# Kernel optimization log

Measured on AMD Instinct MI355X. Metric: run time of the kernel, lower is better.

## Reference

```python
import jax, jax.numpy as jnp
import numpy as np
import math

EMBED_DIM = 1024
NUM_HEADS = 16
PROJ_DIM = 1024
HEAD_DIM = PROJ_DIM // NUM_HEADS  # 64
ALPHA = 0.3  # warmup_steps=0, step_count irrelevant -> alpha_eff = alpha
DIFFUSION_STEPS = 2


def setup_inputs() -> dict:
    key = jax.random.key(0)
    ks = jax.random.split(key, 9)
    B, N, D = 1, 2048, EMBED_DIM
    s_in = 1.0 / math.sqrt(D)
    s_p = 1.0 / math.sqrt(PROJ_DIM)
    return {
        "hidden_states": jax.random.normal(ks[0], (B, N, D), dtype=jnp.float32),
        # Linear weights stored as [in, out] (apply as x @ W + b)
        "Wq": jax.random.normal(ks[1], (D, PROJ_DIM), dtype=jnp.float32) * s_in,
        "bq": jax.random.normal(ks[2], (PROJ_DIM,), dtype=jnp.float32) * s_in,
        "Wk": jax.random.normal(ks[3], (D, PROJ_DIM), dtype=jnp.float32) * s_in,
        "bk": jax.random.normal(ks[4], (PROJ_DIM,), dtype=jnp.float32) * s_in,
        "Wv": jax.random.normal(ks[5], (D, PROJ_DIM), dtype=jnp.float32) * s_in,
        "bv": jax.random.normal(ks[6], (PROJ_DIM,), dtype=jnp.float32) * s_in,
        "Wo": jax.random.normal(ks[7], (PROJ_DIM, D), dtype=jnp.float32) * s_p,
        "bo": jax.random.normal(ks[8], (D,), dtype=jnp.float32) * s_p,
    }


def reference(hidden_states, Wq, bq, Wk, bk, Wv, bv, Wo, bo):
    B, N, D = hidden_states.shape
    H, hd = NUM_HEADS, HEAD_DIM

    def split_heads(x):  # [B, N, P] -> [B, H, N, hd]
        return x.reshape(B, -1, H, hd).transpose(0, 2, 1, 3)

    Q = split_heads(hidden_states @ Wq + bq)
    K = split_heads(hidden_states @ Wk + bk)
    V = split_heads(hidden_states @ Wv + bv)

    # scores: note original uses (sqrt(hd) + 1e-8) denominator here
    scores = jnp.einsum("bhqd,bhkd->bhqk", Q, K) / (math.sqrt(hd) + 1e-8)
    p0 = jax.nn.softmax(scores, axis=-1)

    # key-transition matrix P: exact sqrt(hd) denominator
    sim = jnp.einsum("bhid,bhjd->bhij", K, K) / math.sqrt(hd)
    P = jax.nn.softmax(sim, axis=-1)

    # iterative diffusion, unrolled (early-stop can only fire after the
    # final update when diffusion_steps=2, so output is identical)
    a = ALPHA
    p = p0
    for _ in range(DIFFUSION_STEPS):
        p = (1.0 - a) * p0 + a * jnp.einsum("bhqn,bhnm->bhqm", p, P)

    attn = jnp.einsum("bhqk,bhkd->bhqd", p, V)
    attn = attn.transpose(0, 2, 1, 3).reshape(B, N, PROJ_DIM)
    out = attn @ Wo + bo
    return out, p
```

## Files before the change

### kernel.cpp

```cpp
#include <hip/hip_runtime.h>


typedef __attribute__((ext_vector_type(8))) short bf16x8;
typedef __attribute__((ext_vector_type(4))) short s16x4;
typedef __attribute__((ext_vector_type(4))) float f32x4;

constexpr int N_TOK   = 2048;
constexpr int N_HEADS = 16;
constexpr int HD      = 64;
constexpr int EMB     = 1024;

#define DEVINL __device__ __forceinline__

DEVINL unsigned short f2bf_u(float f) {
  unsigned x = __float_as_uint(f);
  return (unsigned short)((x + 0x7fffu + ((x >> 16) & 1u)) >> 16);
}
DEVINL float bf2f_u(unsigned short h) { return __uint_as_float(((unsigned)h) << 16); }

DEVINL void async16(const void* src, void* dst) {
  __builtin_amdgcn_global_load_lds(
      (const __attribute__((address_space(1))) void*)src,
      (__attribute__((address_space(3))) void*)dst, 16, 0, 0);
}

enum : int { EPI_F32SCALE = 0, EPI_F32BIAS, EPI_BF16, EPI_QKSPLIT, EPI_VSPLIT,
             EPI_DIFF_BF16, EPI_DIFF_F32 };

template<int EPI>
__global__ __launch_bounds__(512, 2)
void gemm256_diff(const unsigned short* __restrict__ Am, int lda, long long sAz,
                  const unsigned short* __restrict__ Bm, int ldb, long long sBz,
                  int K,
                  const unsigned short* __restrict__ P0, int ldp0, long long sPz,
                  void* __restrict__ Cv, int ldc, long long sCz)
{
  __shared__ __align__(16) char smem[2 * 65536];
  const int tid  = threadIdx.x;
  const int lane = tid & 63, wv = tid >> 6;
  const int wr = wv >> 2, wc = wv & 3;
  const int l15 = lane & 15, g = lane >> 4;
  const int z = blockIdx.z;
  const size_t brow = (size_t)blockIdx.y * 256;
  const size_t bcol = (size_t)blockIdx.x * 256;
  const unsigned short* Ab = Am + (size_t)z * (size_t)sAz;
  const unsigned short* Bb = Bm + (size_t)z * (size_t)sBz;
  const int NT = K >> 6;

  const int cbs = (tid & 7) * 16;
  const int r00 = (tid >> 3),       r01 = 64  + (tid >> 3);
  const int r10 = 128 + (tid >> 3), r11 = 192 + (tid >> 3);
  const char* sA00 = (const char*)Ab + ((brow + r00) * (size_t)lda) * 2 + (cbs ^ ((r00 & 7) << 4));
  const char* sA01 = (const char*)Ab + ((brow + r01) * (size_t)lda) * 2 + (cbs ^ ((r01 & 7) << 4));
  const char* sA10 = (const char*)Ab + ((brow + r10) * (size_t)lda) * 2 + (cbs ^ ((r10 & 7) << 4));
  const char* sA11 = (const char*)Ab + ((brow + r11) * (size_t)lda) * 2 + (cbs ^ ((r11 & 7) << 4));
  const char* sB00 = (const char*)Bb + ((bcol + r00) * (size_t)ldb) * 2 + (cbs ^ ((r00 & 7) << 4));
  const char* sB01 = (const char*)Bb + ((bcol + r01) * (size_t)ldb) * 2 + (cbs ^ ((r01 & 7) << 4));
  const char* sB10 = (const char*)Bb + ((bcol + r10) * (size_t)ldb) * 2 + (cbs ^ ((r10 & 7) << 4));
  const char* sB11 = (const char*)Bb + ((bcol + r11) * (size_t)ldb) * 2 + (cbs ^ ((r11 & 7) << 4));

  f32x4 acc[8][4];
  #pragma unroll
  for (int m = 0; m < 8; ++m)
    #pragma unroll
    for (int n = 0; n < 4; ++n) acc[m][n] = f32x4{0.f, 0.f, 0.f, 0.f};

  auto ldA = [&](int cur, int mf, int kk) -> bf16x8 {
    const int row = wr * 128 + mf * 16 + l15;
    const int c = (kk * 64 + g * 16) ^ ((row & 7) << 4);
    return *(const bf16x8*)(smem + cur * 65536 + row * 128 + c);
  };
  auto ldB = [&](int cur, int nf, int kk) -> bf16x8 {
    const int row = wc * 64 + nf * 16 + l15;
    const int c = (kk * 64 + g * 16) ^ ((row & 7) << 4);
    return *(const bf16x8*)(smem + cur * 65536 + 32768 + row * 128 + c);
  };

  {
    char* d0 = smem;
    async16(sA00, d0 +             wv * 1024);
    async16(sA01, d0 +  8192 +     wv * 1024);
    async16(sA10, d0 + 16384 +     wv * 1024);
    async16(sA11, d0 + 24576 +     wv * 1024);
    async16(sB00, d0 + 32768 +     wv * 1024);
    async16(sB01, d0 + 40960 +     wv * 1024);
    async16(sB10, d0 + 49152 +     wv * 1024);
    async16(sB11, d0 + 57344 +     wv * 1024);
    if (NT > 1) {
      char* d1 = smem + 65536 + 32768;
      async16(sB00 + 128, d1 +             wv * 1024);
      async16(sB01 + 128, d1 +  8192 +     wv * 1024);
      async16(sB10 + 128, d1 + 16384 +     wv * 1024);
      async16(sB11 + 128, d1 + 24576 +     wv * 1024);
      asm volatile("s_waitcnt vmcnt(4)" ::: "memory");
    } else {
      asm volatile("s_waitcnt vmcnt(0)" ::: "memory");
    }
    __builtin_amdgcn_sched_barrier(0);
    __builtin_amdgcn_s_barrier();
  }

#define MFMA16(Q)                                                                          \
    __builtin_amdgcn_s_setprio(1);                                                         \
    acc[2*(Q)+0][0] = __builtin_amdgcn_mfma_f32_16x16x32_bf16(a00, b00, acc[2*(Q)+0][0], 0, 0, 0); \
    acc[2*(Q)+0][1] = __builtin_amdgcn_mfma_f32_16x16x32_bf16(a00, b10, acc[2*(Q)+0][1], 0, 0, 0); \
    acc[2*(Q)+0][2] = __builtin_amdgcn_mfma_f32_16x16x32_bf16(a00, b20, acc[2*(Q)+0][2], 0, 0, 0); \
    acc[2*(Q)+0][3] = __builtin_amdgcn_mfma_f32_16x16x32_bf16(a00, b30, acc[2*(Q)+0][3], 0, 0, 0); \
    acc[2*(Q)+1][0] = __builtin_amdgcn_mfma_f32_16x16x32_bf16(a10, b00, acc[2*(Q)+1][0], 0, 0, 0); \
    acc[2*(Q)+1][1] = __builtin_amdgcn_mfma_f32_16x16x32_bf16(a10, b10, acc[2*(Q)+1][1], 0, 0, 0); \
    acc[2*(Q)+1][2] = __builtin_amdgcn_mfma_f32_16x16x32_bf16(a10, b20, acc[2*(Q)+1][2], 0, 0, 0); \
    acc[2*(Q)+1][3] = __builtin_amdgcn_mfma_f32_16x16x32_bf16(a10, b30, acc[2*(Q)+1][3], 0, 0, 0); \
    acc[2*(Q)+0][0] = __builtin_amdgcn_mfma_f32_16x16x32_bf16(a01, b01, acc[2*(Q)+0][0], 0, 0, 0); \
    acc[2*(Q)+0][1] = __builtin_amdgcn_mfma_f32_16x16x32_bf16(a01, b11, acc[2*(Q)+0][1], 0, 0, 0); \
    acc[2*(Q)+0][2] = __builtin_amdgcn_mfma_f32_16x16x32_bf16(a01, b21, acc[2*(Q)+0][2], 0, 0, 0); \
    acc[2*(Q)+0][3] = __builtin_amdgcn_mfma_f32_16x16x32_bf16(a01, b31, acc[2*(Q)+0][3], 0, 0, 0); \
    acc[2*(Q)+1][0] = __builtin_amdgcn_mfma_f32_16x16x32_bf16(a11, b01, acc[2*(Q)+1][0], 0, 0, 0); \
    acc[2*(Q)+1][1] = __builtin_amdgcn_mfma_f32_16x16x32_bf16(a11, b11, acc[2*(Q)+1][1], 0, 0, 0); \
    acc[2*(Q)+1][2] = __builtin_amdgcn_mfma_f32_16x16x32_bf16(a11, b21, acc[2*(Q)+1][2], 0, 0, 0); \
    acc[2*(Q)+1][3] = __builtin_amdgcn_mfma_f32_16x16x32_bf16(a11, b31, acc[2*(Q)+1][3], 0, 0, 0); \
    __builtin_amdgcn_s_setprio(0);

  int cur = 0;
  for (int t = 0; t < NT; ++t, cur ^= 1) {
    const int o = cur ^ 1;
    bf16x8 b00, b01, b10, b11, b20, b21, b30, b31;
    {
      bf16x8 a00 = ldA(cur, 0, 0), a01 = ldA(cur, 0, 1);
      bf16x8 a10 = ldA(cur, 1, 0), a11 = ldA(cur, 1, 1);
      b00 = ldB(cur, 0, 0); b01 = ldB(cur, 0, 1);
      b10 = ldB(cur, 1, 0); b11 = ldB(cur, 1, 1);
      b20 = ldB(cur, 2, 0); b21 = ldB(cur, 2, 1);
      b30 = ldB(cur, 3, 0); b31 = ldB(cur, 3, 1);
      if (t + 1 < NT) {
        char* d = smem + o * 65536;
        const size_t ko = (size_t)(t + 1) * 128;
        async16(sA00 + ko, d +             wv * 1024);
        async16(sA01 + ko, d +  8192 +     wv * 1024);
        async16(sA10 + ko, d + 16384 +     wv * 1024);
        async16(sA11 + ko, d + 24576 +     wv * 1024);
      }
      asm volatile("s_waitcnt lgkmcnt(0)" ::: "memory");
      __builtin_amdgcn_sched_barrier(0);
      __builtin_amdgcn_s_barrier();
      MFMA16(0)
      __builtin_amdgcn_sched_barrier(0);
      __builtin_amdgcn_s_barrier();
    }
    {
      bf16x8 a00 = ldA(cur, 2, 0), a01 = ldA(cur, 2, 1);
      bf16x8 a10 = ldA(cur, 3, 0), a11 = ldA(cur, 3, 1);
      if (t + 2 < NT) {
        char* d = smem + cur * 65536 + 32768;
        const size_t ko = (size_t)(t + 2) * 128;
        async16(sB00 + ko, d +        wv * 1024);
        async16(sB01 + ko, d + 8192 + wv * 1024);
      }
      asm volatile("s_waitcnt lgkmcnt(0)" ::: "memory");
      __builtin_amdgcn_sched_barrier(0);
      __builtin_amdgcn_s_barrier();
      MFMA16(1)
      __builtin_amdgcn_sched_barrier(0);
      __builtin_amdgcn_s_barrier();
    }
    {
      bf16x8 a00 = ldA(cur, 4, 0), a01 = ldA(cur, 4, 1);
      bf16x8 a10 = ldA(cur, 5, 0), a11 = ldA(cur, 5, 1);
      if (t + 2 < NT) {
        char* d = smem + cur * 65536 + 32768 + 16384;
        const size_t ko = (size_t)(t + 2) * 128;
        async16(sB10 + ko, d +        wv * 1024);
        async16(sB11 + ko, d + 8192 + wv * 1024);
      }
      asm volatile("s_waitcnt lgkmcnt(0)" ::: "memory");
      __builtin_amdgcn_sched_barrier(0);
      __builtin_amdgcn_s_barrier();
      MFMA16(2)
      __builtin_amdgcn_sched_barrier(0);
      __builtin_amdgcn_s_barrier();
    }
    {
      bf16x8 a00 = ldA(cur, 6, 0), a01 = ldA(cur, 6, 1);
      bf16x8 a10 = ldA(cur, 7, 0), a11 = ldA(cur, 7, 1);
      asm volatile("s_waitcnt lgkmcnt(0)" ::: "memory");
      __builtin_amdgcn_sched_barrier(0);
      __builtin_amdgcn_s_barrier();
      MFMA16(3)
      if (t + 1 < NT) {
        if (t + 2 < NT) asm volatile("s_waitcnt vmcnt(4)" ::: "memory");
        else            asm volatile("s_waitcnt vmcnt(0)" ::: "memory");
        __builtin_amdgcn_sched_barrier(0);
        __builtin_amdgcn_s_barrier();
      }
    }
  }
#undef MFMA16

  float* Cf = (float*)Cv + (size_t)z * (size_t)sCz;
  unsigned short* Cu = (unsigned short*)Cv + (size_t)z * (size_t)sCz;
  const unsigned short* P0z = P0 + (size_t)z * (size_t)sPz;
  #pragma unroll
  for (int m = 0; m < 8; ++m)
  #pragma unroll
  for (int n = 0; n < 4; ++n)
  #pragma unroll
  for (int j = 0; j < 4; ++j) {
    const size_t R = brow + (size_t)(wr * 128 + m * 16 + g * 4 + j);
    const size_t C = bcol + (size_t)(wc * 64 + n * 16 + l15);
    const float v = acc[m][n][j];
    const float p0v = bf2f_u(P0z[R * (size_t)ldp0 + C]);
    const float r = 0.7f * p0v + 0.3f * v;
    if constexpr (EPI == EPI_DIFF_BF16) Cu[R * ldc + C] = f2bf_u(r);
    else                                Cf[R * ldc + C] = r;
  }
}

template<int BM, int BN, bool AF32, int EPI>
__global__ __launch_bounds__(256)
void gemm_tn(const void* __restrict__ Av, int lda, long long sAz,
             const unsigned short* __restrict__ Bm, int ldb, long long sBz,
             int K, float alpha, const float* __restrict__ bias,
             const unsigned short* __restrict__ P0, int ldp0, long long sPz,
             void* __restrict__ Cv, int ldc, long long sCz)
{
  constexpr int BKk = 64;
  constexpr int WM = BM / 2, WN = BN / 2, MF = WM / 16, NF = WN / 16;
  constexpr int AES = AF32 ? 4 : 2;
  constexpr int ABYTES = BM * BKk * AES, BBYTES = BN * BKk * 2;
  __shared__ __align__(16) char smem[ABYTES + BBYTES];

  const int tid  = threadIdx.x;
  const int lane = tid & 63, wv = tid >> 6;
  const int wr = wv >> 1, wc = wv & 1;
  const int l15 = lane & 15, g = lane >> 4;
  const int z = blockIdx.z;
  const size_t brow = (size_t)blockIdx.y * BM;
  const size_t bcol = (size_t)blockIdx.x * BN;

  const char* Ab = (const char*)Av + (size_t)z * (size_t)sAz * AES;
  const unsigned short* Bb = Bm + (size_t)z * (size_t)sBz;

  f32x4 acc[MF][NF];
  #pragma unroll
  for (int m = 0; m < MF; ++m)
    #pragma unroll
    for (int n = 0; n < NF; ++n)
      acc[m][n] = f32x4{0.f, 0.f, 0.f, 0.f};

  constexpr int EPC_A = AF32 ? 4 : 8;
  constexpr int CPR_A = BKk / EPC_A;
  constexpr int IT_A  = (BM * CPR_A) / 256;
  constexpr int CPR_B = 8;
  constexpr int IT_B  = (BN * CPR_B) / 256;

  for (int k0 = 0; k0 < K; k0 += BKk) {
    #pragma unroll
    for (int i = 0; i < IT_A; ++i) {
      const int c   = i * 256 + wv * 64 + lane;
      const int row = c / CPR_A;
      const int eo  = (c % CPR_A) * EPC_A;
      const char* src = Ab + ((brow + row) * (size_t)lda + (size_t)(k0 + eo)) * AES;
      async16(src, smem + (size_t)(i * 256 + wv * 64) * 16);
    }
    #pragma unroll
    for (int i = 0; i < IT_B; ++i) {
      const int c   = i * 256 + wv * 64 + lane;
      const int row = c / CPR_B;
      const int eo  = (c % CPR_B) * 8;
      const unsigned short* src = Bb + (bcol + row) * (size_t)ldb + (size_t)(k0 + eo);
      async16(src, smem + ABYTES + (size_t)(i * 256 + wv * 64) * 16);
    }
    __syncthreads();
    #pragma unroll
    for (int kk = 0; kk < 2; ++kk) {
      bf16x8 a[MF], b[NF];
      #pragma unroll
      for (int m = 0; m < MF; ++m) {
        const int r = wr * WM + m * 16 + l15;
        if constexpr (!AF32) {
          a[m] = *(const bf16x8*)(smem + ((size_t)r * BKk + kk * 32 + g * 8) * 2);
        } else {
          const float* pa = (const float*)smem + (size_t)r * BKk + kk * 32 + g * 8;
          const f32x4 lo = *(const f32x4*)pa;
          const f32x4 hi = *(const f32x4*)(pa + 4);
          bf16x8 t;
          t[0] = (short)f2bf_u(lo[0]); t[1] = (short)f2bf_u(lo[1]);
          t[2] = (short)f2bf_u(lo[2]); t[3] = (short)f2bf_u(lo[3]);
          t[4] = (short)f2bf_u(hi[0]); t[5] = (short)f2bf_u(hi[1]);
          t[6] = (short)f2bf_u(hi[2]); t[7] = (short)f2bf_u(hi[3]);
          a[m] = t;
        }
      }
      #pragma unroll
      for (int n = 0; n < NF; ++n) {
        const int cc = wc * WN + n * 16 + l15;
        b[n] = *(const bf16x8*)(smem + ABYTES + ((size_t)cc * BKk + kk * 32 + g * 8) * 2);
      }
      #pragma unroll
      for (int m = 0; m < MF; ++m)
        #pragma unroll
        for (int n = 0; n < NF; ++n)
          acc[m][n] = __builtin_amdgcn_mfma_f32_16x16x32_bf16(a[m], b[n], acc[m][n], 0, 0, 0);
    }
    __syncthreads();
  }

  float* Cf = (float*)Cv + (size_t)z * (size_t)sCz;
  unsigned short* Cu = (unsigned short*)Cv + (size_t)z * (size_t)sCz;

  #pragma unroll
  for (int m = 0; m < MF; ++m)
  #pragma unroll
  for (int n = 0; n < NF; ++n)
  #pragma unroll
  for (int j = 0; j < 4; ++j) {
    const size_t R  = brow + (size_t)(wr * WM + m * 16 + g * 4 + j);
    const size_t Cc = bcol + (size_t)(wc * WN + n * 16 + l15);
    const float v = acc[m][n][j];
    if constexpr (EPI == EPI_F32SCALE) {
      Cf[R * ldc + Cc] = v * alpha;
    } else if constexpr (EPI == EPI_F32BIAS) {
      Cf[R * ldc + Cc] = v + bias[Cc];
    } else if constexpr (EPI == EPI_BF16) {
      Cu[R * ldc + Cc] = f2bf_u(v);
    } else if constexpr (EPI == EPI_QKSPLIT) {
      const float t = v + bias[Cc];
      Cu[(Cc >> 6) * ((size_t)N_TOK * HD) + R * HD + (Cc & 63)] = f2bf_u(t);
    } else if constexpr (EPI == EPI_VSPLIT) {
      const float t = v + bias[Cc];
      Cu[(Cc >> 6) * ((size_t)HD * N_TOK) + (Cc & 63) * (size_t)N_TOK + R] = f2bf_u(t);
    } else if constexpr (EPI == EPI_DIFF_BF16) {
      const unsigned short* P0z = P0 + (size_t)z * (size_t)sPz;
      const float p0v = bf2f_u(P0z[R * (size_t)ldp0 + Cc]);
      Cu[R * ldc + Cc] = f2bf_u(0.7f * p0v + 0.3f * v);
    } else if constexpr (EPI == EPI_DIFF_F32) {
      const unsigned short* P0z = P0 + (size_t)z * (size_t)sPz;
      const float p0v = bf2f_u(P0z[R * (size_t)ldp0 + Cc]);
      Cf[R * ldc + Cc] = 0.7f * p0v + 0.3f * v;
    }
  }
  (void)alpha; (void)bias; (void)P0; (void)ldp0;
}

__global__ __launch_bounds__(256)
void row_softmax(const float* __restrict__ S, long long sS,
                 unsigned short* __restrict__ O, long long sO)
{
  __shared__ float red[8];
  const int tid = threadIdx.x;
  const size_t row = blockIdx.x;
  const size_t h = blockIdx.y;
  const f32x4* Sr = (const f32x4*)(S + (size_t)h * sS + row * N_TOK);
  f32x4 v0 = Sr[tid], v1 = Sr[tid + 256];
  float m = fmaxf(fmaxf(fmaxf(v0[0], v0[1]), fmaxf(v0[2], v0[3])),
                  fmaxf(fmaxf(v1[0], v1[1]), fmaxf(v1[2], v1[3])));
  #pragma unroll
  for (int o = 32; o; o >>= 1) m = fmaxf(m, __shfl_xor(m, o));
  if ((tid & 63) == 0) red[tid >> 6] = m;
  __syncthreads();
  m = fmaxf(fmaxf(red[0], red[1]), fmaxf(red[2], red[3]));
  f32x4 e0, e1;
  #pragma unroll
  for (int k = 0; k < 4; ++k) { e0[k] = expf(v0[k] - m); e1[k] = expf(v1[k] - m); }
  float s = e0[0]+e0[1]+e0[2]+e0[3]+e1[0]+e1[1]+e1[2]+e1[3];
  #pragma unroll
  for (int o = 32; o; o >>= 1) s += __shfl_xor(s, o);
  if ((tid & 63) == 0) red[4 + (tid >> 6)] = s;
  __syncthreads();
  s = red[4] + red[5] + red[6] + red[7];
  const float inv = 1.0f / s;
  s16x4 o0, o1;
  #pragma unroll
  for (int k = 0; k < 4; ++k) {
    o0[k] = (short)f2bf_u(e0[k] * inv);
    o1[k] = (short)f2bf_u(e1[k] * inv);
  }
  s16x4* Or = (s16x4*)(O + (size_t)h * sO + row * N_TOK);
  Or[tid] = o0; Or[tid + 256] = o1;
}

__global__ __launch_bounds__(256)
void row_reduce(const float* __restrict__ S, long long sS,
                float* __restrict__ mx, float* __restrict__ is_)
{
  __shared__ float red[8];
  const int tid = threadIdx.x;
  const size_t row = blockIdx.x;
  const size_t h = blockIdx.y;
  const f32x4* Sr = (const f32x4*)(S + (size_t)h * sS + row * N_TOK);
  f32x4 v0 = Sr[tid], v1 = Sr[tid + 256];
  float m = fmaxf(fmaxf(fmaxf(v0[0], v0[1]), fmaxf(v0[2], v0[3])),
                  fmaxf(fmaxf(v1[0], v1[1]), fmaxf(v1[2], v1[3])));
  #pragma unroll
  for (int o = 32; o; o >>= 1) m = fmaxf(m, __shfl_xor(m, o));
  if ((tid & 63) == 0) red[tid >> 6] = m;
  __syncthreads();
  m = fmaxf(fmaxf(red[0], red[1]), fmaxf(red[2], red[3]));
  float s = 0.f;
  #pragma unroll
  for (int k = 0; k < 4; ++k) { s += expf(v0[k] - m); s += expf(v1[k] - m); }
  #pragma unroll
  for (int o = 32; o; o >>= 1) s += __shfl_xor(s, o);
  if ((tid & 63) == 0) red[4 + (tid >> 6)] = s;
  __syncthreads();
  s = red[4] + red[5] + red[6] + red[7];
  if (tid == 0) { mx[h * N_TOK + row] = m; is_[h * N_TOK + row] = 1.0f / s; }
}

__global__ __launch_bounds__(256)
void pt_write(const float* __restrict__ S, long long sS,
              const float* __restrict__ mx, const float* __restrict__ is_,
              unsigned short* __restrict__ PT, long long sP)
{
  const int tid = threadIdx.x;
  const size_t row = blockIdx.x;
  const size_t h = blockIdx.y;
  const f32x4* Sr = (const f32x4*)(S + (size_t)h * sS + row * N_TOK);
  const f32x4* M4 = (const f32x4*)(mx + h * N_TOK);
  const f32x4* I4 = (const f32x4*)(is_ + h * N_TOK);
  s16x4* Pr = (s16x4*)(PT + (size_t)h * sP + row * N_TOK);
  #pragma unroll
  for (int i = 0; i < 2; ++i) {
    const int idx = tid + i * 256;
    f32x4 sv = Sr[idx], mv = M4[idx], iv = I4[idx];
    s16x4 o;
    #pragma unroll
    for (int k = 0; k < 4; ++k) o[k] = (short)f2bf_u(expf(sv[k] - mv[k]) * iv[k]);
    Pr[idx] = o;
  }
}

__global__ __launch_bounds__(256)
void transpose_cast4(const float* __restrict__ w0, const float* __restrict__ w1,
                     const float* __restrict__ w2, const float* __restrict__ w3,
                     unsigned short* __restrict__ o0, unsigned short* __restrict__ o1,
                     unsigned short* __restrict__ o2, unsigned short* __restrict__ o3)
{
  __shared__ float tile[64][65];
  const float* in; unsigned short* out;
  if      (blockIdx.z == 0) { in = w0; out = o0; }
  else if (blockIdx.z == 1) { in = w1; out = o1; }
  else if (blockIdx.z == 2) { in = w2; out = o2; }
  else                      { in = w3; out = o3; }
  const int n = EMB;
  const int bx = blockIdx.x * 64, by = blockIdx.y * 64;
  const int tid = threadIdx.x;
  const int r = tid >> 2;
  const int q = tid & 3;
  #pragma unroll
  for (int i = 0; i < 4; ++i) {
    const int c = q * 16 + i * 4;
    f32x4 v = *(const f32x4*)(in + (size_t)(by + r) * n + bx + c);
    tile[r][c + 0] = v[0]; tile[r][c + 1] = v[1];
    tile[r][c + 2] = v[2]; tile[r][c + 3] = v[3];
  }
  __syncthreads();
  #pragma unroll
  for (int i = 0; i < 4; ++i) {
    const int c0 = q * 16 + i * 4;
    s16x4 o;
    o[0] = (short)f2bf_u(tile[c0 + 0][r]); o[1] = (short)f2bf_u(tile[c0 + 1][r]);
    o[2] = (short)f2bf_u(tile[c0 + 2][r]); o[3] = (short)f2bf_u(tile[c0 + 3][r]);
    *(s16x4*)(out + (size_t)(bx + r) * n + by + c0) = o;
  }
}

__global__ __launch_bounds__(256)
void cast_f32_bf16(const float* __restrict__ in, unsigned short* __restrict__ out)
{
  const size_t i = (size_t)blockIdx.x * 256 + threadIdx.x;
  f32x4 v = ((const f32x4*)in)[i];
  s16x4 o;
  o[0] = (short)f2bf_u(v[0]); o[1] = (short)f2bf_u(v[1]);
  o[2] = (short)f2bf_u(v[2]); o[3] = (short)f2bf_u(v[3]);
  ((s16x4*)out)[i] = o;
}

extern "C" void kernel_launch(void* const* d_in, const int* in_sizes, int n_in,
                              void* d_out, int out_size, void* d_ws, size_t ws_size,
                              hipStream_t stream)
{
  (void)in_sizes; (void)n_in; (void)out_size;
  const float* hs = (const float*)d_in[0];
  const float* Wq = (const float*)d_in[1];
  const float* bq = (const float*)d_in[2];
  const float* Wk = (const float*)d_in[3];
  const float* bk = (const float*)d_in[4];
  const float* Wv = (const float*)d_in[5];
  const float* bv = (const float*)d_in[6];
  const float* Wo = (const float*)d_in[7];
  const float* bo = (const float*)d_in[8];

  float* outO = (float*)d_out;
  float* outP = outO + (size_t)N_TOK * EMB;

  const long long NN = (long long)N_TOK * N_TOK;

  const bool batched = ws_size >= ((size_t)440 << 20);
  const int PH = batched ? N_HEADS : 1;

  char* ws = (char*)d_ws;
  auto alloc = [&](size_t b) { char* p = ws; ws += (b + 255) & ~(size_t)255; return p; };
  unsigned short* Xbf = (unsigned short*)alloc((size_t)N_TOK * EMB * 2);
  unsigned short* WqT = (unsigned short*)alloc((size_t)EMB * EMB * 2);
  unsigned short* WkT = (unsigned short*)alloc((size_t)EMB * EMB * 2);
  unsigned short* WvT = (unsigned short*)alloc((size_t)EMB * EMB * 2);
  unsigned short* WoT = (unsigned short*)alloc((size_t)EMB * EMB * 2);
  unsigned short* Qb  = (unsigned short*)alloc((size_t)N_HEADS * N_TOK * HD * 2);
  unsigned short* Kb  = (unsigned short*)alloc((size_t)N_HEADS * N_TOK * HD * 2);
  unsigned short* Vt  = (unsigned short*)alloc((size_t)N_HEADS * N_TOK * HD * 2);
  unsigned short* attn= (unsigned short*)alloc((size_t)N_TOK * EMB * 2);
  float* mx  = (float*)alloc((size_t)PH * N_TOK * 4);
  float* is_ = (float*)alloc((size_t)PH * N_TOK * 4);
  unsigned short* p0b = (unsigned short*)alloc((size_t)PH * NN * 2);
  unsigned short* PT  = (unsigned short*)alloc((size_t)PH * NN * 2);
  unsigned short* p1b = (unsigned short*)alloc((size_t)PH * NN * 2);

  cast_f32_bf16<<<dim3(N_TOK * EMB / 1024), 256, 0, stream>>>(hs, Xbf);
  transpose_cast4<<<dim3(16, 16, 4), 256, 0, stream>>>(Wq, Wk, Wv, Wo, WqT, WkT, WvT, WoT);

  gemm_tn<128, 128, false, EPI_QKSPLIT><<<dim3(EMB / 128, N_TOK / 128, 1), 256, 0, stream>>>(
      Xbf, EMB, 0, WqT, EMB, 0, EMB, 0.f, bq, nullptr, 0, 0, Qb, 0, 0);
  gemm_tn<128, 128, false, EPI_QKSPLIT><<<dim3(EMB / 128, N_TOK / 128, 1), 256, 0, stream>>>(
      Xbf, EMB, 0, WkT, EMB, 0, EMB, 0.f, bk, nullptr, 0, 0, Kb, 0, 0);
  gemm_tn<128, 128, false, EPI_VSPLIT><<<dim3(EMB / 128, N_TOK / 128, 1), 256, 0, stream>>>(
      Xbf, EMB, 0, WvT, EMB, 0, EMB, 0.f, bv, nullptr, 0, 0, Vt, 0, 0);

  if (batched) {
    const long long sH = (long long)N_TOK * HD;
    gemm_tn<128, 128, false, EPI_F32SCALE><<<dim3(16, 16, N_HEADS), 256, 0, stream>>>(
        Qb, HD, sH, Kb, HD, sH, HD, 0.125f, nullptr, nullptr, 0, 0, outP, N_TOK, NN);
    row_softmax<<<dim3(N_TOK, N_HEADS), 256, 0, stream>>>(outP, NN, p0b, NN);
    gemm_tn<128, 128, false, EPI_F32SCALE><<<dim3(16, 16, N_HEADS), 256, 0, stream>>>(
        Kb, HD, sH, Kb, HD, sH, HD, 0.125f, nullptr, nullptr, 0, 0, outP, N_TOK, NN);
    row_reduce<<<dim3(N_TOK, N_HEADS), 256, 0, stream>>>(outP, NN, mx, is_);
    pt_write<<<dim3(N_TOK, N_HEADS), 256, 0, stream>>>(outP, NN, mx, is_, PT, NN);
    gemm256_diff<EPI_DIFF_BF16><<<dim3(8, 8, N_HEADS), 512, 0, stream>>>(
        p0b, N_TOK, NN, PT, N_TOK, NN, N_TOK, p0b, N_TOK, NN, p1b, N_TOK, NN);
    gemm256_diff<EPI_DIFF_F32><<<dim3(8, 8, N_HEADS), 512, 0, stream>>>(
        p1b, N_TOK, NN, PT, N_TOK, NN, N_TOK, p0b, N_TOK, NN, outP, N_TOK, NN);
  } else {
    for (int h = 0; h < N_HEADS; ++h) {
      float* slot = outP + (size_t)h * NN;
      const unsigned short* Qh = Qb + (size_t)h * N_TOK * HD;
      const unsigned short* Kh = Kb + (size_t)h * N_TOK * HD;
      gemm_tn<128, 128, false, EPI_F32SCALE><<<dim3(16, 16, 1), 256, 0, stream>>>(
          Qh, HD, 0, Kh, HD, 0, HD, 0.125f, nullptr, nullptr, 0, 0, slot, N_TOK, 0);
      row_softmax<<<dim3(N_TOK, 1), 256, 0, stream>>>(slot, 0, p0b, 0);
      gemm_tn<128, 128, false, EPI_F32SCALE><<<dim3(16, 16, 1), 256, 0, stream>>>(
          Kh, HD, 0, Kh, HD, 0, HD, 0.125f, nullptr, nullptr, 0, 0, slot, N_TOK, 0);
      row_reduce<<<dim3(N_TOK, 1), 256, 0, stream>>>(slot, 0, mx, is_);
      pt_write<<<dim3(N_TOK, 1), 256, 0, stream>>>(slot, 0, mx, is_, PT, 0);
      gemm_tn<128, 128, false, EPI_DIFF_BF16><<<dim3(16, 16, 1), 256, 0, stream>>>(
          p0b, N_TOK, 0, PT, N_TOK, 0, N_TOK, 0.f, nullptr, p0b, N_TOK, 0, p1b, N_TOK, 0);
      gemm_tn<128, 128, false, EPI_DIFF_F32><<<dim3(16, 16, 1), 256, 0, stream>>>(
          p1b, N_TOK, 0, PT, N_TOK, 0, N_TOK, 0.f, nullptr, p0b, N_TOK, 0, slot, N_TOK, 0);
    }
  }

  gemm_tn<128, 64, true, EPI_BF16><<<dim3(1, N_TOK / 128, N_HEADS), 256, 0, stream>>>(
      outP, N_TOK, NN, Vt, N_TOK, (long long)HD * N_TOK,
      N_TOK, 0.f, nullptr, nullptr, 0, 0, attn, EMB, HD);

  gemm_tn<128, 128, false, EPI_F32BIAS><<<dim3(EMB / 128, N_TOK / 128, 1), 256, 0, stream>>>(
      attn, EMB, 0, WoT, EMB, 0, EMB, 0.f, bo, nullptr, 0, 0, outO, EMB, 0);
}
```

Before: 1.105 ms.

## Emit bf16 copy of diffused probabilities, swizzle block order, respread async loads

The final diffusion GEMM now writes both the fp32 probability output and a bf16 copy, so the PV GEMM reads half-width bf16 instead of converting from fp32. Block indices are remapped with a flat swizzle to improve cache locality across tiles and heads. Async global-to-LDS loads for the next A and B tiles are spread evenly over the four MFMA phases, and the barrier and wait placement is reordered. The batched path now needs more workspace for the extra buffer; if the workspace is too small, execution falls back to the slower per-head loop.

```diff
diff --git a/kernel.cpp b/kernel.cpp
--- a/kernel.cpp
+++ b/kernel.cpp
@@ -25,7 +25,7 @@
 }
 
 enum : int { EPI_F32SCALE = 0, EPI_F32BIAS, EPI_BF16, EPI_QKSPLIT, EPI_VSPLIT,
-             EPI_DIFF_BF16, EPI_DIFF_F32 };
+             EPI_DIFF_BF16, EPI_DIFF_F32, EPI_DIFF_BOTH };
 
 template<int EPI>
 __global__ __launch_bounds__(512, 2)
@@ -33,16 +33,21 @@
                   const unsigned short* __restrict__ Bm, int ldb, long long sBz,
                   int K,
                   const unsigned short* __restrict__ P0, int ldp0, long long sPz,
-                  void* __restrict__ Cv, int ldc, long long sCz)
+                  void* __restrict__ Cv, int ldc, long long sCz,
+                  unsigned short* __restrict__ C2)
 {
   __shared__ __align__(16) char smem[2 * 65536];
   const int tid  = threadIdx.x;
   const int lane = tid & 63, wv = tid >> 6;
   const int wr = wv >> 2, wc = wv & 3;
   const int l15 = lane & 15, g = lane >> 4;
-  const int z = blockIdx.z;
-  const size_t brow = (size_t)blockIdx.y * 256;
-  const size_t bcol = (size_t)blockIdx.x * 256;
+
+  const int flat = blockIdx.z * 64 + blockIdx.y * 8 + blockIdx.x;
+  const int swz  = (flat & 7) * 128 + (flat >> 3);
+  const int z    = swz >> 6;
+  const size_t brow = (size_t)((swz >> 3) & 7) * 256;
+  const size_t bcol = (size_t)(swz & 7) * 256;
+
   const unsigned short* Ab = Am + (size_t)z * (size_t)sAz;
   const unsigned short* Bb = Bm + (size_t)z * (size_t)sBz;
   const int NT = K >> 6;
@@ -123,6 +128,8 @@
   int cur = 0;
   for (int t = 0; t < NT; ++t, cur ^= 1) {
     const int o = cur ^ 1;
+    const size_t ko1 = (size_t)(t + 1) * 128;
+    const size_t ko2 = (size_t)(t + 2) * 128;
     bf16x8 b00, b01, b10, b11, b20, b21, b30, b31;
     {
       bf16x8 a00 = ldA(cur, 0, 0), a01 = ldA(cur, 0, 1);
@@ -133,15 +140,14 @@
       b30 = ldB(cur, 3, 0); b31 = ldB(cur, 3, 1);
       if (t + 1 < NT) {
         char* d = smem + o * 65536;
-        const size_t ko = (size_t)(t + 1) * 128;
-        async16(sA00 + ko, d +             wv * 1024);
-        async16(sA01 + ko, d +  8192 +     wv * 1024);
-        async16(sA10 + ko, d + 16384 +     wv * 1024);
-        async16(sA11 + ko, d + 24576 +     wv * 1024);
-      }
+        async16(sA00 + ko1, d +        wv * 1024);
+        async16(sA01 + ko1, d + 8192 + wv * 1024);
+      }
+      asm volatile("s_waitcnt lgkmcnt(8)" ::: "memory");
+      __builtin_amdgcn_sched_barrier(0);
+      __builtin_amdgcn_s_barrier();
       asm volatile("s_waitcnt lgkmcnt(0)" ::: "memory");
       __builtin_amdgcn_sched_barrier(0);
-      __builtin_amdgcn_s_barrier();
       MFMA16(0)
       __builtin_amdgcn_sched_barrier(0);
       __builtin_amdgcn_s_barrier();
@@ -149,15 +155,15 @@
     {
       bf16x8 a00 = ldA(cur, 2, 0), a01 = ldA(cur, 2, 1);
       bf16x8 a10 = ldA(cur, 3, 0), a11 = ldA(cur, 3, 1);
-      if (t + 2 < NT) {
-        char* d = smem + cur * 65536 + 32768;
-        const size_t ko = (size_t)(t + 2) * 128;
-        async16(sB00 + ko, d +        wv * 1024);
-        async16(sB01 + ko, d + 8192 + wv * 1024);
-      }
+      if (t + 1 < NT) {
+        char* d = smem + o * 65536;
+        async16(sA10 + ko1, d + 16384 + wv * 1024);
+        async16(sA11 + ko1, d + 24576 + wv * 1024);
+      }
+      __builtin_amdgcn_sched_barrier(0);
+      __builtin_amdgcn_s_barrier();
       asm volatile("s_waitcnt lgkmcnt(0)" ::: "memory");
       __builtin_amdgcn_sched_barrier(0);
-      __builtin_amdgcn_s_barrier();
       MFMA16(1)
       __builtin_amdgcn_sched_barrier(0);
       __builtin_amdgcn_s_barrier();
@@ -166,14 +172,14 @@
       bf16x8 a00 = ldA(cur, 4, 0), a01 = ldA(cur, 4, 1);
       bf16x8 a10 = ldA(cur, 5, 0), a11 = ldA(cur, 5, 1);
       if (t + 2 < NT) {
-        char* d = smem + cur * 65536 + 32768 + 16384;
-        const size_t ko = (size_t)(t + 2) * 128;
-        async16(sB10 + ko, d +        wv * 1024);
-        async16(sB11 + ko, d + 8192 + wv * 1024);
-      }
+        char* d = smem + cur * 65536 + 32768;
+        async16(sB00 + ko2, d +        wv * 1024);
+        async16(sB01 + ko2, d + 8192 + wv * 1024);
+      }
+      __builtin_amdgcn_sched_barrier(0);
+      __builtin_amdgcn_s_barrier();
       asm volatile("s_waitcnt lgkmcnt(0)" ::: "memory");
       __builtin_amdgcn_sched_barrier(0);
-      __builtin_amdgcn_s_barrier();
       MFMA16(2)
       __builtin_amdgcn_sched_barrier(0);
       __builtin_amdgcn_s_barrier();
@@ -181,9 +187,15 @@
     {
       bf16x8 a00 = ldA(cur, 6, 0), a01 = ldA(cur, 6, 1);
       bf16x8 a10 = ldA(cur, 7, 0), a11 = ldA(cur, 7, 1);
+      if (t + 2 < NT) {
+        char* d = smem + cur * 65536 + 32768 + 16384;
+        async16(sB10 + ko2, d +        wv * 1024);
+        async16(sB11 + ko2, d + 8192 + wv * 1024);
+      }
+      __builtin_amdgcn_sched_barrier(0);
+      __builtin_amdgcn_s_barrier();
       asm volatile("s_waitcnt lgkmcnt(0)" ::: "memory");
       __builtin_amdgcn_sched_barrier(0);
-      __builtin_amdgcn_s_barrier();
       MFMA16(3)
       if (t + 1 < NT) {
         if (t + 2 < NT) asm volatile("s_waitcnt vmcnt(4)" ::: "memory");
@@ -197,6 +209,7 @@
 
   float* Cf = (float*)Cv + (size_t)z * (size_t)sCz;
   unsigned short* Cu = (unsigned short*)Cv + (size_t)z * (size_t)sCz;
+  unsigned short* Cu2 = C2 ? C2 + (size_t)z * (size_t)sCz : nullptr;
   const unsigned short* P0z = P0 + (size_t)z * (size_t)sPz;
   #pragma unroll
   for (int m = 0; m < 8; ++m)
@@ -209,8 +222,14 @@
     const float v = acc[m][n][j];
     const float p0v = bf2f_u(P0z[R * (size_t)ldp0 + C]);
     const float r = 0.7f * p0v + 0.3f * v;
-    if constexpr (EPI == EPI_DIFF_BF16) Cu[R * ldc + C] = f2bf_u(r);
-    else                                Cf[R * ldc + C] = r;
+    if constexpr (EPI == EPI_DIFF_BF16) {
+      Cu[R * ldc + C] = f2bf_u(r);
+    } else if constexpr (EPI == EPI_DIFF_BOTH) {
+      Cf[R * ldc + C] = r;
+      Cu2[R * ldc + C] = f2bf_u(r);
+    } else {
+      Cf[R * ldc + C] = r;
+    }
   }
 }
 
@@ -495,7 +514,7 @@
 
   const long long NN = (long long)N_TOK * N_TOK;
 
-  const bool batched = ws_size >= ((size_t)440 << 20);
+  const bool batched = ws_size >= ((size_t)600 << 20);
   const int PH = batched ? N_HEADS : 1;
 
   char* ws = (char*)d_ws;
@@ -514,6 +533,7 @@
   unsigned short* p0b = (unsigned short*)alloc((size_t)PH * NN * 2);
   unsigned short* PT  = (unsigned short*)alloc((size_t)PH * NN * 2);
   unsigned short* p1b = (unsigned short*)alloc((size_t)PH * NN * 2);
+  unsigned short* p2b = batched ? (unsigned short*)alloc((size_t)PH * NN * 2) : nullptr;
 
   cast_f32_bf16<<<dim3(N_TOK * EMB / 1024), 256, 0, stream>>>(hs, Xbf);
   transpose_cast4<<<dim3(16, 16, 4), 256, 0, stream>>>(Wq, Wk, Wv, Wo, WqT, WkT, WvT, WoT);
@@ -535,9 +555,12 @@
     row_reduce<<<dim3(N_TOK, N_HEADS), 256, 0, stream>>>(outP, NN, mx, is_);
     pt_write<<<dim3(N_TOK, N_HEADS), 256, 0, stream>>>(outP, NN, mx, is_, PT, NN);
     gemm256_diff<EPI_DIFF_BF16><<<dim3(8, 8, N_HEADS), 512, 0, stream>>>(
-        p0b, N_TOK, NN, PT, N_TOK, NN, N_TOK, p0b, N_TOK, NN, p1b, N_TOK, NN);
-    gemm256_diff<EPI_DIFF_F32><<<dim3(8, 8, N_HEADS), 512, 0, stream>>>(
-        p1b, N_TOK, NN, PT, N_TOK, NN, N_TOK, p0b, N_TOK, NN, outP, N_TOK, NN);
+        p0b, N_TOK, NN, PT, N_TOK, NN, N_TOK, p0b, N_TOK, NN, p1b, N_TOK, NN, nullptr);
+    gemm256_diff<EPI_DIFF_BOTH><<<dim3(8, 8, N_HEADS), 512, 0, stream>>>(
+        p1b, N_TOK, NN, PT, N_TOK, NN, N_TOK, p0b, N_TOK, NN, outP, N_TOK, NN, p2b);
+    gemm_tn<128, 64, false, EPI_BF16><<<dim3(1, N_TOK / 128, N_HEADS), 256, 0, stream>>>(
+        p2b, N_TOK, NN, Vt, N_TOK, (long long)HD * N_TOK,
+        N_TOK, 0.f, nullptr, nullptr, 0, 0, attn, EMB, HD);
   } else {
     for (int h = 0; h < N_HEADS; ++h) {
       float* slot = outP + (size_t)h * NN;
@@ -555,11 +578,10 @@
       gemm_tn<128, 128, false, EPI_DIFF_F32><<<dim3(16, 16, 1), 256, 0, stream>>>(
           p1b, N_TOK, 0, PT, N_TOK, 0, N_TOK, 0.f, nullptr, p0b, N_TOK, 0, slot, N_TOK, 0);
     }
-  }
-
-  gemm_tn<128, 64, true, EPI_BF16><<<dim3(1, N_TOK / 128, N_HEADS), 256, 0, stream>>>(
-      outP, N_TOK, NN, Vt, N_TOK, (long long)HD * N_TOK,
-      N_TOK, 0.f, nullptr, nullptr, 0, 0, attn, EMB, HD);
+    gemm_tn<128, 64, true, EPI_BF16><<<dim3(1, N_TOK / 128, N_HEADS), 256, 0, stream>>>(
+        outP, N_TOK, NN, Vt, N_TOK, (long long)HD * N_TOK,
+        N_TOK, 0.f, nullptr, nullptr, 0, 0, attn, EMB, HD);
+  }
 
   gemm_tn<128, 128, false, EPI_F32BIAS><<<dim3(EMB / 128, N_TOK / 128, 1), 256, 0, stream>>>(
       attn, EMB, 0, WoT, EMB, 0, EMB, 0.f, bo, nullptr, 0, 0, outO, EMB, 0);
```

Result: no change. 1.119 ms (+1.2%).
